# Kernel optimization log

Measured on AMD Instinct MI355X. Metric: run time of the kernel, lower is better.

## Reference

```python
import jax, jax.numpy as jnp
import numpy as np

INPUT_SIZE = 20
HIDDEN = 51
OUT = 1
B = 4096
T = 512


def _init_lstm_params(key, in_dim, hid_dim):
    # PyTorch LSTMCell init: U(-1/sqrt(hid), 1/sqrt(hid))
    k = 1.0 / np.sqrt(hid_dim)
    ks = jax.random.split(key, 4)
    W_ih = jax.random.uniform(ks[0], (4 * hid_dim, in_dim), minval=-k, maxval=k, dtype=jnp.float32)
    W_hh = jax.random.uniform(ks[1], (4 * hid_dim, hid_dim), minval=-k, maxval=k, dtype=jnp.float32)
    b_ih = jax.random.uniform(ks[2], (4 * hid_dim,), minval=-k, maxval=k, dtype=jnp.float32)
    b_hh = jax.random.uniform(ks[3], (4 * hid_dim,), minval=-k, maxval=k, dtype=jnp.float32)
    return W_ih, W_hh, b_ih, b_hh


def setup_inputs() -> dict:
    key = jax.random.key(0)
    k_x, k1, k2, k3, k4 = jax.random.split(key, 5)
    x = jax.random.normal(k_x, (B, T, INPUT_SIZE), dtype=jnp.float32)
    W_ih1, W_hh1, b_ih1, b_hh1 = _init_lstm_params(k1, INPUT_SIZE, HIDDEN)
    W_ih2, W_hh2, b_ih2, b_hh2 = _init_lstm_params(k2, HIDDEN, OUT)
    kl = 1.0 / np.sqrt(OUT)
    ka, kb, kc, kd = jax.random.split(k3, 4)
    W_mu = jax.random.uniform(ka, (OUT, OUT), minval=-kl, maxval=kl, dtype=jnp.float32)
    b_mu = jax.random.uniform(kb, (OUT,), minval=-kl, maxval=kl, dtype=jnp.float32)
    W_lv = jax.random.uniform(kc, (OUT, OUT), minval=-kl, maxval=kl, dtype=jnp.float32)
    b_lv = jax.random.uniform(kd, (OUT,), minval=-kl, maxval=kl, dtype=jnp.float32)
    return {
        "x": x,
        "W_ih1": W_ih1, "W_hh1": W_hh1, "b_ih1": b_ih1, "b_hh1": b_hh1,
        "W_ih2": W_ih2, "W_hh2": W_hh2, "b_ih2": b_ih2, "b_hh2": b_hh2,
        "W_mu": W_mu, "b_mu": b_mu, "W_lv": W_lv, "b_lv": b_lv,
    }


def _lstm_cell(x_t, h, c, W_ih, W_hh, b_ih, b_hh):
    # PyTorch LSTMCell: gate order i, f, g, o
    gates = x_t @ W_ih.T + b_ih + h @ W_hh.T + b_hh
    i, f, g, o = jnp.split(gates, 4, axis=-1)
    c_new = jax.nn.sigmoid(f) * c + jax.nn.sigmoid(i) * jnp.tanh(g)
    h_new = jax.nn.sigmoid(o) * jnp.tanh(c_new)
    return h_new, c_new


def reference(x, W_ih1, W_hh1, b_ih1, b_hh1, W_ih2, W_hh2, b_ih2, b_hh2, W_mu, b_mu, W_lv, b_lv):
    bsz = x.shape[0]
    h1 = jnp.zeros((bsz, HIDDEN), dtype=x.dtype)
    c1 = jnp.zeros((bsz, HIDDEN), dtype=x.dtype)
    h2 = jnp.zeros((bsz, OUT), dtype=x.dtype)
    c2 = jnp.zeros((bsz, OUT), dtype=x.dtype)

    def step(carry, x_t):
        h1, c1, h2, c2 = carry
        h1, c1 = _lstm_cell(x_t, h1, c1, W_ih1, W_hh1, b_ih1, b_hh1)
        h2, c2 = _lstm_cell(h1, h2, c2, W_ih2, W_hh2, b_ih2, b_hh2)
        return (h1, c1, h2, c2), h2

    xs = jnp.swapaxes(x, 0, 1)  # [T, B, input_size]
    _, h2_seq = jax.lax.scan(step, (h1, c1, h2, c2), xs)  # h2_seq: [T, B, 1]
    agg = jnp.mean(h2_seq, axis=0)  # [B, 1] mean over time
    mu = agg @ W_mu.T + b_mu
    log_var = agg @ W_lv.T + b_lv
    sigma = jnp.exp(0.5 * log_var)
    lower = mu - 1.96 * sigma
    upper = mu + 1.96 * sigma
    return (lower, mu, upper, log_var)
```

## Files before the change

kernel.cpp:

```cpp
#include <hip/hip_runtime.h>

#define B_TOT 4096
#define T_STEPS 512
#define IN 20
#define HID 51

typedef float f32x4 __attribute__((ext_vector_type(4)));
typedef short s16x8 __attribute__((ext_vector_type(8)));

__device__ __forceinline__ unsigned short f2bf(float f) {
    unsigned int u = __float_as_uint(f);
    unsigned int r = (u + 0x7fffu + ((u >> 16) & 1u)) >> 16;
    return (unsigned short)r;
}

#define L2E  1.4426950408889634f
#define L2E2 2.8853900817779268f

__device__ __forceinline__ float fast_rcp(float x) { return __builtin_amdgcn_rcpf(x); }
__device__ __forceinline__ float ex2(float x)      { return __builtin_amdgcn_exp2f(x); }
__device__ __forceinline__ float sig_p(float p)  { return fast_rcp(1.0f + ex2(p)); }
__device__ __forceinline__ float tanh_q(float q) { return 1.0f - 2.0f * fast_rcp(1.0f + ex2(q)); }
__device__ __forceinline__ float tanh2_q(float q) {
    return __builtin_fmaf(fast_rcp(1.0f + ex2(q)), -2.0f * L2E2, L2E2);
}


__global__ __launch_bounds__(512, 2)
void lstm_fused(const float* __restrict__ x,
                const float* __restrict__ Wih1, const float* __restrict__ Whh1,
                const float* __restrict__ bih1, const float* __restrict__ bhh1,
                const float* __restrict__ Wih2, const float* __restrict__ Whh2,
                const float* __restrict__ bih2, const float* __restrict__ bhh2,
                const float* __restrict__ Wmu,  const float* __restrict__ bmu,
                const float* __restrict__ Wlv,  const float* __restrict__ blv,
                float* __restrict__ out)
{
    __shared__ __align__(16) unsigned short vA[2][2][64][8];
    __shared__ __align__(16) unsigned short xS[4][64][8];

    const int tid  = threadIdx.x;
    const int lane = tid & 63;
    const int w    = tid >> 6;
    const int bidx = blockIdx.x;

    const int tbase = (w == 0) ? 0 : (w == 7) ? 12 : 2 * w - 1;
    const int ntile = (w >= 1 && w <= 5) ? 2 : 1;
    const bool isST = (w == 0);
    const bool isL2 = (w == 6);

    s16x8 wfrag[2][3];
    f32x4 binit[2];
    #pragma unroll
    for (int ti = 0; ti < 2; ++ti) {
        const int tau = tbase + ti;
        const int m = lane & 15;
        const bool act = (ti < ntile);
        #pragma unroll
        for (int ks = 0; ks < 3; ++ks) {
            s16x8 f;
            #pragma unroll
            for (int j = 0; j < 8; ++j) {
                int k = ks * 32 + ((lane >> 4) << 3) + j;
                float v = 0.0f;
                if (act) {
                    int g = m & 3, unit = tau * 4 + (m >> 2);
                    if (unit < HID) {
                        int row = g * HID + unit;
                        if (k < IN) v = Wih1[row * IN + k];
                        else if (k >= 32 && k < 32 + HID) v = Whh1[row * HID + (k - 32)];
                        v *= (g == 2) ? L2E2 : -L2E;
                    }
                }
                f[j] = (short)f2bf(v);
            }
            wfrag[ti][ks] = f;
        }
        f32x4 bi = {0.f, 0.f, 0.f, 0.f};
        if (act) {
            int unit = tau * 4 + (lane >> 4);
            if (unit < HID) {
                #pragma unroll
                for (int r = 0; r < 4; ++r)
                    bi[r] = (bih1[r * HID + unit] + bhh1[r * HID + unit]) * ((r == 2) ? L2E2 : -L2E);
            }
        }
        binit[ti] = bi;
    }

    s16x8 l2frag[2];
    f32x4 l2binit = {0.f, 0.f, 0.f, 0.f};
    float whh2g[4] = {0.f, 0.f, 0.f, 0.f};
    if (isL2) {
        const int m = lane & 15;
        #pragma unroll
        for (int ks = 1; ks < 3; ++ks) {
            s16x8 f;
            #pragma unroll
            for (int j = 0; j < 8; ++j) {
                int k = ks * 32 + ((lane >> 4) << 3) + j;
                float v = 0.0f;
                if (m < 4 && k >= 32 && k < 32 + HID)
                    v = Wih2[m * HID + (k - 32)] * ((m == 2) ? L2E2 : -L2E);
                f[j] = (short)f2bf(v);
            }
            l2frag[ks - 1] = f;
        }
        #pragma unroll
        for (int r = 0; r < 4; ++r) {
            float s = (r == 2) ? L2E2 : -L2E;
            whh2g[r]   = Whh2[r] * s;
            l2binit[r] = (bih2[r] + bhh2[r]) * s;
        }
    }

    const float* sp[5];
    int srow[5], sj[5];
    if (isST) {
        #pragma unroll
        for (int i = 0; i < 5; ++i) {
            int e = i * 64 + lane;
            int b = e / IN, m = e % IN;
            sp[i]   = x + ((size_t)(bidx * 16 + b) * T_STEPS) * IN + m;
            srow[i] = ((m >> 3) & 3) * 16 + b;
            sj[i]   = m & 7;
        }
    }

    {
        unsigned short* vz = &vA[0][0][0][0];
        for (int i = tid; i < 2 * 2 * 64 * 8; i += 512) vz[i] = 0;
        unsigned short* xz = &xS[0][0][0];
        for (int i = tid; i < 4 * 64 * 8; i += 512) xz[i] = 0;
    }
    __syncthreads();
    float rE[5], rO[5];
    if (isST) {
        #pragma unroll
        for (int i = 0; i < 5; ++i) {
            xS[0][srow[i]][sj[i]] = f2bf(sp[i][0]);
            xS[1][srow[i]][sj[i]] = f2bf(sp[i][IN]);
            rE[i] = sp[i][(size_t)2 * IN];
            rO[i] = sp[i][(size_t)3 * IN];
        }
    }
    __syncthreads();

    f32x4 accx[2];
    {
        const s16x8 b00 = *(const s16x8*)&xS[0][lane][0];
        #pragma unroll
        for (int ti = 0; ti < 2; ++ti)
            accx[ti] = __builtin_amdgcn_mfma_f32_16x16x32_bf16(wfrag[ti][0], b00, binit[ti], 0, 0, 0);
    }

    float C1[2] = {0.f, 0.f};
    float C2p = 0.f, h2p = 0.f, sum2 = 0.f;

#define STEP(tt, P, XR, XW, XREG)                                                \
    {                                                                            \
        if (isST) {                                                              \
            const int t4 = ((tt) < T_STEPS - 4) ? (tt) + 4 : T_STEPS - 1;        \
            _Pragma("unroll")                                                    \
            for (int i = 0; i < 5; ++i) {                                        \
                xS[XW][srow[i]][sj[i]] = f2bf(XREG[i]);                          \
                XREG[i] = sp[i][(size_t)t4 * IN];                                \
            }                                                                    \
        }                                                                        \
        const s16x8 bf1 = *(const s16x8*)&vA[P][0][lane][0];                     \
        const s16x8 bf2 = *(const s16x8*)&vA[P][1][lane][0];                     \
        _Pragma("unroll")                                                        \
        for (int ti = 0; ti < 2; ++ti) {                                         \
            if (ti < ntile) {                                                    \
                f32x4 a = accx[ti];                                              \
                a = __builtin_amdgcn_mfma_f32_16x16x32_bf16(wfrag[ti][1], bf1, a, 0, 0, 0); \
                a = __builtin_amdgcn_mfma_f32_16x16x32_bf16(wfrag[ti][2], bf2, a, 0, 0, 0); \
                float C = sig_p(a[1]) * C1[ti] + sig_p(a[0]) * tanh2_q(a[2]);    \
                C1[ti] = C;                                                      \
                float h = sig_p(a[3]) * tanh_q(C);                               \
                int unit = (tbase + ti) * 4 + (lane >> 4);                       \
                int k    = 32 + unit;                                            \
                int b    = lane & 15;                                            \
                vA[(P) ^ 1][(k >> 5) - 1][(((k >> 3) & 3) << 4) + b][k & 7] = f2bf(h); \
            }                                                                    \
        }                                                                        \
        if (isL2) {                                                              \
            f32x4 a = l2binit;                                                   \
            a = __builtin_amdgcn_mfma_f32_16x16x32_bf16(l2frag[0], bf1, a, 0, 0, 0); \
            a = __builtin_amdgcn_mfma_f32_16x16x32_bf16(l2frag[1], bf2, a, 0, 0, 0); \
            if ((tt) > 0 && lane < 16) {                                         \
                float pi = a[0] + whh2g[0] * h2p;                                \
                float pf = a[1] + whh2g[1] * h2p;                                \
                float pg = a[2] + whh2g[2] * h2p;                                \
                float po = a[3] + whh2g[3] * h2p;                                \
                float C2 = sig_p(pf) * C2p + sig_p(pi) * tanh2_q(pg);            \
                C2p = C2;                                                        \
                h2p = sig_p(po) * tanh_q(C2);                                    \
                sum2 += h2p;                                                     \
            }                                                                    \
        }                                                                        \
        {   \
            const s16x8 bf0n = *(const s16x8*)&xS[XR][lane][0];                  \
            _Pragma("unroll")                                                    \
            for (int ti = 0; ti < 2; ++ti)                                       \
                accx[ti] = __builtin_amdgcn_mfma_f32_16x16x32_bf16(wfrag[ti][0], bf0n, binit[ti], 0, 0, 0); \
        }                                                                        \
        __syncthreads();                                                         \
    }

    for (int t = 0; t < T_STEPS; t += 4) {
        STEP(t + 0, 0, 1, 2, rE)
        STEP(t + 1, 1, 2, 3, rO)
        STEP(t + 2, 0, 3, 0, rE)
        STEP(t + 3, 1, 0, 1, rO)
    }
#undef STEP

    if (isL2) {
        s16x8 bf1 = *(const s16x8*)&vA[0][0][lane][0];
        s16x8 bf2 = *(const s16x8*)&vA[0][1][lane][0];
        f32x4 a = l2binit;
        a = __builtin_amdgcn_mfma_f32_16x16x32_bf16(l2frag[0], bf1, a, 0, 0, 0);
        a = __builtin_amdgcn_mfma_f32_16x16x32_bf16(l2frag[1], bf2, a, 0, 0, 0);
        if (lane < 16) {
            float pi = a[0] + whh2g[0] * h2p;
            float pf = a[1] + whh2g[1] * h2p;
            float pg = a[2] + whh2g[2] * h2p;
            float po = a[3] + whh2g[3] * h2p;
            float C2 = sig_p(pf) * C2p + sig_p(pi) * tanh2_q(pg);
            h2p = sig_p(po) * tanh_q(C2);
            sum2 += h2p;

            float agg = sum2 * (1.0f / 512.0f);
            float mu  = Wmu[0] * agg + bmu[0];
            float lv  = Wlv[0] * agg + blv[0];
            float sg  = __expf(0.5f * lv);
            int bg = bidx * 16 + lane;
            out[bg]             = mu - 1.96f * sg;
            out[B_TOT + bg]     = mu;
            out[2 * B_TOT + bg] = mu + 1.96f * sg;
            out[3 * B_TOT + bg] = lv;
        }
    }
}

extern "C" void kernel_launch(void* const* d_in, const int* in_sizes, int n_in,
                              void* d_out, int out_size, void* d_ws, size_t ws_size,
                              hipStream_t stream) {
    const float* x    = (const float*)d_in[0];
    const float* Wih1 = (const float*)d_in[1];
    const float* Whh1 = (const float*)d_in[2];
    const float* bih1 = (const float*)d_in[3];
    const float* bhh1 = (const float*)d_in[4];
    const float* Wih2 = (const float*)d_in[5];
    const float* Whh2 = (const float*)d_in[6];
    const float* bih2 = (const float*)d_in[7];
    const float* bhh2 = (const float*)d_in[8];
    const float* Wmu  = (const float*)d_in[9];
    const float* bmu  = (const float*)d_in[10];
    const float* Wlv  = (const float*)d_in[11];
    const float* blv  = (const float*)d_in[12];
    float* out = (float*)d_out;

    lstm_fused<<<dim3(B_TOT / 16), dim3(512), 0, stream>>>(
        x, Wih1, Whh1, bih1, bhh1, Wih2, Whh2, bih2, bhh2, Wmu, bmu, Wlv, blv, out);
}
```

Measured before the change: 449.9 us.

## Free layer-2 warp from tile work and defer its cell update one step

Reassigns the layer-1 gate tiles so warp 6, which runs layer 2, no longer owns any layer-1 tile; warp 7 picks up the extra tile. The layer-2 cell update now uses the MFMA result from the previous step, held in a register, and runs at the start of the next step, so its transcendental work overlaps the other warps' layer-1 work instead of lengthening the critical path before the barrier. Input-projection MFMAs are skipped for inactive tiles. This adds a one-step-deeper pipeline with an extra epilogue step and reindexed tile ownership, which must still cover all 13 tiles correctly.

```diff
diff --git a/kernel.cpp b/kernel.cpp
--- a/kernel.cpp
+++ b/kernel.cpp
@@ -44,8 +44,8 @@
     const int w    = tid >> 6;
     const int bidx = blockIdx.x;
 
-    const int tbase = (w == 0) ? 0 : (w == 7) ? 12 : 2 * w - 1;
-    const int ntile = (w >= 1 && w <= 5) ? 2 : 1;
+    const int tbase = (w == 0) ? 0 : (w == 7) ? 11 : (w == 6) ? 0 : 2 * w - 1;
+    const int ntile = (w == 0) ? 1 : (w == 6) ? 0 : 2;
     const bool isST = (w == 0);
     const bool isL2 = (w == 6);
 
@@ -151,11 +151,13 @@
         const s16x8 b00 = *(const s16x8*)&xS[0][lane][0];
         #pragma unroll
         for (int ti = 0; ti < 2; ++ti)
-            accx[ti] = __builtin_amdgcn_mfma_f32_16x16x32_bf16(wfrag[ti][0], b00, binit[ti], 0, 0, 0);
+            if (ti < ntile)
+                accx[ti] = __builtin_amdgcn_mfma_f32_16x16x32_bf16(wfrag[ti][0], b00, binit[ti], 0, 0, 0);
     }
 
     float C1[2] = {0.f, 0.f};
     float C2p = 0.f, h2p = 0.f, sum2 = 0.f;
+    f32x4 aP = l2binit;
 
 #define STEP(tt, P, XR, XW, XREG)                                                \
     {                                                                            \
@@ -169,6 +171,19 @@
         }                                                                        \
         const s16x8 bf1 = *(const s16x8*)&vA[P][0][lane][0];                     \
         const s16x8 bf2 = *(const s16x8*)&vA[P][1][lane][0];                     \
+         \
+        if (isL2) {                                                              \
+            if ((tt) >= 2 && lane < 16) {                                        \
+                float pi = aP[0] + whh2g[0] * h2p;                               \
+                float pf = aP[1] + whh2g[1] * h2p;                               \
+                float pg = aP[2] + whh2g[2] * h2p;                               \
+                float po = aP[3] + whh2g[3] * h2p;                               \
+                float C2 = sig_p(pf) * C2p + sig_p(pi) * tanh2_q(pg);            \
+                C2p = C2;                                                        \
+                h2p = sig_p(po) * tanh_q(C2);                                    \
+                sum2 += h2p;                                                     \
+            }                                                                    \
+        }                                                                        \
         _Pragma("unroll")                                                        \
         for (int ti = 0; ti < 2; ++ti) {                                         \
             if (ti < ntile) {                                                    \
@@ -184,26 +199,18 @@
                 vA[(P) ^ 1][(k >> 5) - 1][(((k >> 3) & 3) << 4) + b][k & 7] = f2bf(h); \
             }                                                                    \
         }                                                                        \
-        if (isL2) {                                                              \
+        if (isL2) {             \
             f32x4 a = l2binit;                                                   \
             a = __builtin_amdgcn_mfma_f32_16x16x32_bf16(l2frag[0], bf1, a, 0, 0, 0); \
             a = __builtin_amdgcn_mfma_f32_16x16x32_bf16(l2frag[1], bf2, a, 0, 0, 0); \
-            if ((tt) > 0 && lane < 16) {                                         \
-                float pi = a[0] + whh2g[0] * h2p;                                \
-                float pf = a[1] + whh2g[1] * h2p;                                \
-                float pg = a[2] + whh2g[2] * h2p;                                \
-                float po = a[3] + whh2g[3] * h2p;                                \
-                float C2 = sig_p(pf) * C2p + sig_p(pi) * tanh2_q(pg);            \
-                C2p = C2;                                                        \
-                h2p = sig_p(po) * tanh_q(C2);                                    \
-                sum2 += h2p;                                                     \
-            }                                                                    \
-        }                                                                        \
-        {   \
+            aP = a;                                                              \
+        }                                                                        \
+        if (ntile > 0) {      \
             const s16x8 bf0n = *(const s16x8*)&xS[XR][lane][0];                  \
             _Pragma("unroll")                                                    \
             for (int ti = 0; ti < 2; ++ti)                                       \
-                accx[ti] = __builtin_amdgcn_mfma_f32_16x16x32_bf16(wfrag[ti][0], bf0n, binit[ti], 0, 0, 0); \
+                if (ti < ntile)                                                  \
+                    accx[ti] = __builtin_amdgcn_mfma_f32_16x16x32_bf16(wfrag[ti][0], bf0n, binit[ti], 0, 0, 0); \
         }                                                                        \
         __syncthreads();                                                         \
     }
@@ -217,6 +224,16 @@
 #undef STEP
 
     if (isL2) {
+        if (lane < 16) {
+            float pi = aP[0] + whh2g[0] * h2p;
+            float pf = aP[1] + whh2g[1] * h2p;
+            float pg = aP[2] + whh2g[2] * h2p;
+            float po = aP[3] + whh2g[3] * h2p;
+            float C2 = sig_p(pf) * C2p + sig_p(pi) * tanh2_q(pg);
+            C2p = C2;
+            h2p = sig_p(po) * tanh_q(C2);
+            sum2 += h2p;
+        }
         s16x8 bf1 = *(const s16x8*)&vA[0][0][lane][0];
         s16x8 bf2 = *(const s16x8*)&vA[0][1][lane][0];
         f32x4 a = l2binit;
```

After: 467.1 us. +3.8%, slower.

## Assign one gate tile per wavefront using 1024-thread blocks

Applied to the files above, without the earlier changes.

Moves from 8 waves with up to two gate tiles each to 16 waves: 13 waves each own one 4-unit gate tile, plus a dedicated x-staging wave and a layer-2 wave. This shortens each wave's serial chain of MFMA plus activation math per timestep, which bounds the latency of each barrier-separated step. In exchange, block size doubles, so fewer blocks can be resident per CU, and the per-step __syncthreads now spans 16 waves.

```diff
diff --git a/kernel.cpp b/kernel.cpp
--- a/kernel.cpp
+++ b/kernel.cpp
@@ -26,7 +26,7 @@
 }
 
 
-__global__ __launch_bounds__(512, 2)
+__global__ __launch_bounds__(1024)
 void lstm_fused(const float* __restrict__ x,
                 const float* __restrict__ Wih1, const float* __restrict__ Whh1,
                 const float* __restrict__ bih1, const float* __restrict__ bhh1,
@@ -44,18 +44,14 @@
     const int w    = tid >> 6;
     const int bidx = blockIdx.x;
 
-    const int tbase = (w == 0) ? 0 : (w == 7) ? 12 : 2 * w - 1;
-    const int ntile = (w >= 1 && w <= 5) ? 2 : 1;
-    const bool isST = (w == 0);
-    const bool isL2 = (w == 6);
-
-    s16x8 wfrag[2][3];
-    f32x4 binit[2];
-    #pragma unroll
-    for (int ti = 0; ti < 2; ++ti) {
-        const int tau = tbase + ti;
+    const bool isT  = (w <= 12);
+    const bool isST = (w == 13);
+    const bool isL2 = (w == 14);
+
+    s16x8 wfrag[3];
+    f32x4 binit = {0.f, 0.f, 0.f, 0.f};
+    {
         const int m = lane & 15;
-        const bool act = (ti < ntile);
         #pragma unroll
         for (int ks = 0; ks < 3; ++ks) {
             s16x8 f;
@@ -63,8 +59,8 @@
             for (int j = 0; j < 8; ++j) {
                 int k = ks * 32 + ((lane >> 4) << 3) + j;
                 float v = 0.0f;
-                if (act) {
-                    int g = m & 3, unit = tau * 4 + (m >> 2);
+                if (isT) {
+                    int g = m & 3, unit = w * 4 + (m >> 2);
                     if (unit < HID) {
                         int row = g * HID + unit;
                         if (k < IN) v = Wih1[row * IN + k];
@@ -74,18 +70,25 @@
                 }
                 f[j] = (short)f2bf(v);
             }
-            wfrag[ti][ks] = f;
-        }
-        f32x4 bi = {0.f, 0.f, 0.f, 0.f};
-        if (act) {
-            int unit = tau * 4 + (lane >> 4);
+            wfrag[ks] = f;
+        }
+        if (isT) {
+            int unit = w * 4 + (lane >> 4);
             if (unit < HID) {
                 #pragma unroll
                 for (int r = 0; r < 4; ++r)
-                    bi[r] = (bih1[r * HID + unit] + bhh1[r * HID + unit]) * ((r == 2) ? L2E2 : -L2E);
+                    binit[r] = (bih1[r * HID + unit] + bhh1[r * HID + unit]) * ((r == 2) ? L2E2 : -L2E);
             }
         }
-        binit[ti] = bi;
+    }
+
+    int hchunk = 0, hrow = 0, hj = 0;
+    if (isT) {
+        int unit = w * 4 + (lane >> 4);
+        int k    = 32 + unit;
+        hchunk = (k >> 5) - 1;
+        hrow   = (((k >> 3) & 3) << 4) + (lane & 15);
+        hj     = k & 7;
     }
 
     s16x8 l2frag[2];
@@ -129,9 +132,9 @@
 
     {
         unsigned short* vz = &vA[0][0][0][0];
-        for (int i = tid; i < 2 * 2 * 64 * 8; i += 512) vz[i] = 0;
+        for (int i = tid; i < 2 * 2 * 64 * 8; i += 1024) vz[i] = 0;
         unsigned short* xz = &xS[0][0][0];
-        for (int i = tid; i < 4 * 64 * 8; i += 512) xz[i] = 0;
+        for (int i = tid; i < 4 * 64 * 8; i += 1024) xz[i] = 0;
     }
     __syncthreads();
     float rE[5], rO[5];
@@ -146,15 +149,13 @@
     }
     __syncthreads();
 
-    f32x4 accx[2];
-    {
+    f32x4 accx = {0.f, 0.f, 0.f, 0.f};
+    if (isT) {
         const s16x8 b00 = *(const s16x8*)&xS[0][lane][0];
-        #pragma unroll
-        for (int ti = 0; ti < 2; ++ti)
-            accx[ti] = __builtin_amdgcn_mfma_f32_16x16x32_bf16(wfrag[ti][0], b00, binit[ti], 0, 0, 0);
-    }
-
-    float C1[2] = {0.f, 0.f};
+        accx = __builtin_amdgcn_mfma_f32_16x16x32_bf16(wfrag[0], b00, binit, 0, 0, 0);
+    }
+
+    float C1t = 0.f;
     float C2p = 0.f, h2p = 0.f, sum2 = 0.f;
 
 #define STEP(tt, P, XR, XW, XREG)                                                \
@@ -167,24 +168,22 @@
                 XREG[i] = sp[i][(size_t)t4 * IN];                                \
             }                                                                    \
         }                                                                        \
-        const s16x8 bf1 = *(const s16x8*)&vA[P][0][lane][0];                     \
-        const s16x8 bf2 = *(const s16x8*)&vA[P][1][lane][0];                     \
-        _Pragma("unroll")                                                        \
-        for (int ti = 0; ti < 2; ++ti) {                                         \
-            if (ti < ntile) {                                                    \
-                f32x4 a = accx[ti];                                              \
-                a = __builtin_amdgcn_mfma_f32_16x16x32_bf16(wfrag[ti][1], bf1, a, 0, 0, 0); \
-                a = __builtin_amdgcn_mfma_f32_16x16x32_bf16(wfrag[ti][2], bf2, a, 0, 0, 0); \
-                float C = sig_p(a[1]) * C1[ti] + sig_p(a[0]) * tanh2_q(a[2]);    \
-                C1[ti] = C;                                                      \
-                float h = sig_p(a[3]) * tanh_q(C);                               \
-                int unit = (tbase + ti) * 4 + (lane >> 4);                       \
-                int k    = 32 + unit;                                            \
-                int b    = lane & 15;                                            \
-                vA[(P) ^ 1][(k >> 5) - 1][(((k >> 3) & 3) << 4) + b][k & 7] = f2bf(h); \
-            }                                                                    \
+        if (isT) {                                                               \
+            const s16x8 bf1 = *(const s16x8*)&vA[P][0][lane][0];                 \
+            const s16x8 bf2 = *(const s16x8*)&vA[P][1][lane][0];                 \
+            f32x4 a = accx;                                                      \
+            a = __builtin_amdgcn_mfma_f32_16x16x32_bf16(wfrag[1], bf1, a, 0, 0, 0); \
+            a = __builtin_amdgcn_mfma_f32_16x16x32_bf16(wfrag[2], bf2, a, 0, 0, 0); \
+            float C = sig_p(a[1]) * C1t + sig_p(a[0]) * tanh2_q(a[2]);           \
+            C1t = C;                                                             \
+            float h = sig_p(a[3]) * tanh_q(C);                                   \
+            vA[(P) ^ 1][hchunk][hrow][hj] = f2bf(h);                             \
+            const s16x8 bf0n = *(const s16x8*)&xS[XR][lane][0];                  \
+            accx = __builtin_amdgcn_mfma_f32_16x16x32_bf16(wfrag[0], bf0n, binit, 0, 0, 0); \
         }                                                                        \
         if (isL2) {                                                              \
+            const s16x8 bf1 = *(const s16x8*)&vA[P][0][lane][0];                 \
+            const s16x8 bf2 = *(const s16x8*)&vA[P][1][lane][0];                 \
             f32x4 a = l2binit;                                                   \
             a = __builtin_amdgcn_mfma_f32_16x16x32_bf16(l2frag[0], bf1, a, 0, 0, 0); \
             a = __builtin_amdgcn_mfma_f32_16x16x32_bf16(l2frag[1], bf2, a, 0, 0, 0); \
@@ -198,12 +197,6 @@
                 h2p = sig_p(po) * tanh_q(C2);                                    \
                 sum2 += h2p;                                                     \
             }                                                                    \
-        }                                                                        \
-        {   \
-            const s16x8 bf0n = *(const s16x8*)&xS[XR][lane][0];                  \
-            _Pragma("unroll")                                                    \
-            for (int ti = 0; ti < 2; ++ti)                                       \
-                accx[ti] = __builtin_amdgcn_mfma_f32_16x16x32_bf16(wfrag[ti][0], bf0n, binit[ti], 0, 0, 0); \
         }                                                                        \
         __syncthreads();                                                         \
     }
@@ -262,6 +255,6 @@
     const float* blv  = (const float*)d_in[12];
     float* out = (float*)d_out;
 
-    lstm_fused<<<dim3(B_TOT / 16), dim3(512), 0, stream>>>(
+    lstm_fused<<<dim3(B_TOT / 16), dim3(1024), 0, stream>>>(
         x, Wih1, Whh1, bih1, bhh1, Wih2, Whh2, bih2, bhh2, Wmu, bmu, Wlv, blv, out);
 }
```

New measurement: 428.5 us. 1.05x faster.
